# Optimization experiments

Measured on AMD Instinct MI355X. Metric: run time of the kernel, lower is better.

The kernel has to match this reference:

```python
import jax, jax.numpy as jnp
import numpy as np

B, R, T = 32, 256, 4096  # shots, receivers, time samples; P = T prob grid
EPS = 1e-8


def _trapz(y, t):
    # trapezoidal integral along last axis
    dt = t[1:] - t[:-1]
    return jnp.sum(0.5 * (y[..., 1:] + y[..., :-1]) * dt, axis=-1)


def _cum_trap(y, t):
    # cumulative trapezoid along last axis, prepend 0 -> same length as y
    dt = t[1:] - t[:-1]
    incr = 0.5 * (y[..., 1:] + y[..., :-1]) * dt
    c = jnp.cumsum(incr, axis=-1)
    return jnp.concatenate([jnp.zeros_like(c[..., :1]), c], axis=-1)


def _renorm(x, t):
    # square + trapz-normalize each trace to a probability density over t
    pdf = x * x + EPS
    return pdf / _trapz(pdf, t)[..., None]


def setup_inputs() -> dict:
    key = jax.random.key(0)
    k1, k2 = jax.random.split(key)
    traces = 0.5 * jax.random.normal(k1, (B, R, T), dtype=jnp.float32)
    t = jnp.arange(T, dtype=jnp.float32) * 1e-3
    p = jnp.linspace(0.0, 1.0, T, dtype=jnp.float32)  # probability grid
    # q_raw = true_quantile(obs_data, t, p): invert the observed CDF per trace
    obs = 0.5 * jax.random.normal(k2, (B, R, T), dtype=jnp.float32)
    obs_pdf = _renorm(obs, t)
    obs_cdf = _cum_trap(obs_pdf, t)  # strictly increasing (pdf > 0)
    q_raw = jax.vmap(lambda c: jnp.interp(p, c, t))(obs_cdf.reshape(-1, T))
    q_raw = q_raw.reshape(B, R, T).astype(jnp.float32)
    return {"traces": traces, "t": t, "p": p, "q_raw": q_raw}


def reference(traces, t, p, q_raw):
    pdf = _renorm(traces, t)          # [B,R,T]
    cdf = _cum_trap(pdf, t)           # [B,R,T], in [0,1]
    # quantile lookup: interpolate each trace's quantile table at its cdf values
    cdf_f = cdf.reshape(-1, T)
    q_f = q_raw.reshape(-1, T)
    transport = jax.vmap(jnp.interp, in_axes=(0, None, 0))(cdf_f, p, q_f)
    transport = transport.reshape(pdf.shape)
    diff = t - transport
    loss = jnp.sum(_trapz(diff * diff * pdf, t))
    return loss
```

## Files before the change

### kernel.cpp

```cpp
#include <hip/hip_runtime.h>

#define TT 4096
#define BLK 256
#define PER 16
#define EPSV 1e-8f

__device__ __forceinline__ void async_q16(const float* g, float* l) {
  __builtin_amdgcn_global_load_lds(
      (const __attribute__((address_space(1))) void*)g,
      (__attribute__((address_space(3))) void*)l, 16, 0, 0);
}

__global__ __launch_bounds__(BLK) void w2_loss_kernel(
    const float* __restrict__ traces,
    const float* __restrict__ q_raw,
    float* __restrict__ part) {
  __shared__ float qb[TT];
  __shared__ float wave_sums[4];
  __shared__ float wave_red[4];

  const int tid = threadIdx.x;
  const int wv = tid >> 6;
  const int lane = tid & 63;
  const long trace = blockIdx.x;
  const float* __restrict__ tr = traces + trace * (long)TT;
  const float* __restrict__ qr = q_raw + trace * (long)TT;
  const int base = tid * PER;

  float4 trv[4];
  {
    const float4* tr4 = (const float4*)(tr + base);
#pragma unroll
    for (int j = 0; j < 4; ++j) trv[j] = tr4[j];
  }
  float nb = (tid < BLK - 1) ? tr[base + PER] : 0.0f;

#pragma unroll
  for (int j = 0; j < 4; ++j) {
    const int c = (wv * 4 + j) * 256;
    async_q16(qr + c + lane * 4, &qb[c]);
  }

  float s[PER + 1];
#pragma unroll
  for (int j = 0; j < 4; ++j) {
    s[4 * j + 0] = trv[j].x * trv[j].x + EPSV;
    s[4 * j + 1] = trv[j].y * trv[j].y + EPSV;
    s[4 * j + 2] = trv[j].z * trv[j].z + EPSV;
    s[4 * j + 3] = trv[j].w * trv[j].w + EPSV;
  }
  s[PER] = (tid < BLK - 1) ? (nb * nb + EPSV) : 0.0f;

  float lc[PER + 1];
  lc[0] = 0.0f;
  {
    float t0 = (float)base * 1e-3f;
#pragma unroll
    for (int m = 0; m < PER; ++m) {
      float t1 = (float)(base + m + 1) * 1e-3f;
      float incr = 0.5f * (s[m] + s[m + 1]) * (t1 - t0);
      if (m == PER - 1) incr = (tid < BLK - 1) ? incr : 0.0f;
      lc[m + 1] = lc[m] + incr;
      t0 = t1;
    }
  }
  const float tot = lc[PER];

  float v = tot;
#pragma unroll
  for (int off = 1; off < 64; off <<= 1) {
    float n = __shfl_up(v, off, 64);
    if (lane >= off) v += n;
  }
  if (lane == 63) wave_sums[wv] = v;
  __syncthreads();

  float wave_off = 0.0f;
  if (wv > 0) wave_off += wave_sums[0];
  if (wv > 1) wave_off += wave_sums[1];
  if (wv > 2) wave_off += wave_sums[2];
  const float excl = (v - tot) + wave_off;
  const float norm = wave_sums[0] + wave_sums[1] + wave_sums[2] + wave_sums[3];
  const float inv_norm = 1.0f / norm;

  float local = 0.0f;
  {
    float tlo = (tid == 0) ? 0.0f : (float)(base - 1) * 1e-3f;
    float tm = (float)base * 1e-3f;
#pragma unroll
    for (int g = 0; g < 2; ++g) {
      int idx[8];
      float ff[8];
#pragma unroll
      for (int mm = 0; mm < 8; ++mm) {
        const int m = 8 * g + mm;
        float x = (excl + lc[m]) * inv_norm;
        float u = x * (float)(TT - 1);
        int i0 = (int)u;
        i0 = (i0 > TT - 2) ? TT - 2 : i0;
        float f = u - (float)i0;
        idx[mm] = i0;
        ff[mm] = fminf(f, 1.0f);
      }
      float q0v[8], q1v[8];
#pragma unroll
      for (int mm = 0; mm < 8; ++mm) {
        q0v[mm] = qb[idx[mm]];
        q1v[mm] = qb[idx[mm] + 1];
      }
#pragma unroll
      for (int mm = 0; mm < 8; ++mm) {
        const int m = 8 * g + mm;
        float thi = (float)(base + m + 1) * 1e-3f;
        float thi_w = thi;
        if (m == PER - 1) thi_w = (tid == BLK - 1) ? tm : thi;
        float transport = q0v[mm] + ff[mm] * (q1v[mm] - q0v[mm]);
        float d = tm - transport;
        float w = 0.5f * (thi_w - tlo);
        local += d * d * s[m] * w;
        tlo = tm;
        tm = thi;
      }
    }
  }
  local *= inv_norm;

#pragma unroll
  for (int off = 32; off > 0; off >>= 1) local += __shfl_down(local, off, 64);
  if (lane == 0) wave_red[wv] = local;
  __syncthreads();
  if (tid == 0) {
    part[blockIdx.x] = wave_red[0] + wave_red[1] + wave_red[2] + wave_red[3];
  }
}

__global__ __launch_bounds__(BLK) void reduce_kernel(
    const float* __restrict__ part, float* __restrict__ out, int n) {
  __shared__ float wave_red[4];
  const int tid = threadIdx.x;
  float local = 0.0f;
  for (int i = tid; i < n; i += BLK) local += part[i];
#pragma unroll
  for (int off = 32; off > 0; off >>= 1) local += __shfl_down(local, off, 64);
  if ((tid & 63) == 0) wave_red[tid >> 6] = local;
  __syncthreads();
  if (tid == 0) out[0] = wave_red[0] + wave_red[1] + wave_red[2] + wave_red[3];
}

extern "C" void kernel_launch(void* const* d_in, const int* in_sizes, int n_in,
                              void* d_out, int out_size, void* d_ws, size_t ws_size,
                              hipStream_t stream) {
  const float* traces = (const float*)d_in[0];
  const float* q_raw  = (const float*)d_in[3];
  float* out = (float*)d_out;
  float* part = (float*)d_ws;

  const int n_traces = in_sizes[0] / TT;
  w2_loss_kernel<<<n_traces, BLK, 0, stream>>>(traces, q_raw, part);
  reduce_kernel<<<1, BLK, 0, stream>>>(part, out, n_traces);
}
```

Before: 282.7 us.

## Stage traces through swizzled LDS and gather quantiles directly from global

Trace data is now loaded with coalesced float4 reads into a swizzled shared-memory buffer, then redistributed to each thread's contiguous 16-element segment, replacing strided per-thread vector loads. The async copy of the quantile table into LDS is removed, and the interpolation gathers read q_raw directly from global memory (through the caches). This trades a full-table LDS staging for data-dependent global gathers and adds a block barrier before compute.

```diff
diff --git a/kernel.cpp b/kernel.cpp
--- a/kernel.cpp
+++ b/kernel.cpp
@@ -5,17 +5,15 @@
 #define PER 16
 #define EPSV 1e-8f
 
-__device__ __forceinline__ void async_q16(const float* g, float* l) {
-  __builtin_amdgcn_global_load_lds(
-      (const __attribute__((address_space(1))) void*)g,
-      (__attribute__((address_space(3))) void*)l, 16, 0, 0);
+__device__ __forceinline__ int swzf(int a) {
+  return a ^ (((a >> 5) & 7) << 2);
 }
 
 __global__ __launch_bounds__(BLK) void w2_loss_kernel(
     const float* __restrict__ traces,
     const float* __restrict__ q_raw,
     float* __restrict__ part) {
-  __shared__ float qb[TT];
+  __shared__ float ltr[TT];
   __shared__ float wave_sums[4];
   __shared__ float wave_red[4];
 
@@ -27,18 +25,28 @@
   const float* __restrict__ qr = q_raw + trace * (long)TT;
   const int base = tid * PER;
 
+  {
+    const float4* tr4 = (const float4*)tr;
+    float4 pk[4];
+#pragma unroll
+    for (int j = 0; j < 4; ++j) pk[j] = tr4[256 * wv + 64 * j + lane];
+#pragma unroll
+    for (int j = 0; j < 4; ++j) {
+      const int A = (256 * wv + 64 * j + lane) * 4;
+      *(float4*)&ltr[swzf(A)] = pk[j];
+    }
+  }
+  __syncthreads();
+
+  const int swb = ((tid >> 1) & 7) << 2;
   float4 trv[4];
-  {
-    const float4* tr4 = (const float4*)(tr + base);
 #pragma unroll
-    for (int j = 0; j < 4; ++j) trv[j] = tr4[j];
-  }
-  float nb = (tid < BLK - 1) ? tr[base + PER] : 0.0f;
-
-#pragma unroll
-  for (int j = 0; j < 4; ++j) {
-    const int c = (wv * 4 + j) * 256;
-    async_q16(qr + c + lane * 4, &qb[c]);
+  for (int j = 0; j < 4; ++j)
+    trv[j] = *(const float4*)&ltr[(base + 4 * j) ^ swb];
+  float nb = 0.0f;
+  if (tid < BLK - 1) {
+    const int a = base + PER;
+    nb = ltr[swzf(a)];
   }
 
   float s[PER + 1];
@@ -105,8 +113,8 @@
       float q0v[8], q1v[8];
 #pragma unroll
       for (int mm = 0; mm < 8; ++mm) {
-        q0v[mm] = qb[idx[mm]];
-        q1v[mm] = qb[idx[mm] + 1];
+        q0v[mm] = qr[idx[mm]];
+        q1v[mm] = qr[idx[mm] + 1];
       }
 #pragma unroll
       for (int mm = 0; mm < 8; ++mm) {
```

Result: slower. 288.8 us (+2.2%).
